# Kernel tuning notes

Hardware: AMD Instinct MI355X
Metric: run time of the kernel (lower is better)

The kernel has to match this reference:

```python
import jax, jax.numpy as jnp
import numpy as np

SOM = (32, 32)   # som_dim; SOM[0]*SOM[1] == num_embeddings
LR = 0.05


def setup_inputs() -> dict:
    key = jax.random.key(0)
    k1, k2 = jax.random.split(key)
    B, K, D = 65536, 1024, 256
    x = jax.random.normal(k1, (B, D), dtype=jnp.float32)
    embeddings = jax.random.uniform(k2, (K, D), dtype=jnp.float32)  # torch.rand init
    return {"x": x, "embeddings": embeddings}


def reference(x, embeddings):
    K, D = embeddings.shape
    # pairwise squared distances: [B, K]
    dist = (jnp.sum(x * x, axis=1, keepdims=True)
            + jnp.sum(embeddings * embeddings, axis=1)
            - 2.0 * (x @ embeddings.T))
    n_min = jnp.argmin(dist, axis=1)          # [B]
    z_q = embeddings[n_min]                   # [B, D]

    # SOM grid coordinates and clamped neighbors
    n_x = n_min // SOM[1]
    n_y = n_min % SOM[1]
    x_up = jnp.where(n_x < SOM[0] - 1, n_x + 1, n_x)
    x_down = jnp.where(n_x > 0, n_x - 1, n_x)
    y_right = jnp.where(n_y < SOM[1] - 1, n_y + 1, n_y)
    y_left = jnp.where(n_y > 0, n_y - 1, n_y)
    idx_up = x_up * SOM[1] + n_y
    idx_down = x_down * SOM[1] + n_y
    idx_right = n_x * SOM[1] + y_right
    idx_left = n_x * SOM[1] + y_left

    # [B, 4, D] neighbor gather (order: up, down, left, right as in torch code)
    nbr_idx = jnp.stack([idx_up, idx_down, idx_left, idx_right], axis=1)
    z_q_neighbors = embeddings[nbr_idx]

    # SOM scatter update (torch does one-hot matmuls; segment_sum is the fused form)
    dw = x - z_q                              # [B, D]
    seg = lambda idx: jax.ops.segment_sum(dw, idx, num_segments=K)
    new_embeddings = jax.lax.stop_gradient(
        embeddings
        + LR * seg(n_min)
        + 0.5 * LR * (seg(idx_up) + seg(idx_down) + seg(idx_right) + seg(idx_left))
    )

    commit_loss = jnp.mean((x - z_q) ** 2)
    som_loss = jnp.mean((jax.lax.stop_gradient(x)[:, None, :] - z_q_neighbors) ** 2)
    return z_q, commit_loss, som_loss, new_embeddings
```

## Files before the change

kernel.cpp:

```cpp
#include <hip/hip_runtime.h>

#define B_ROWS 65536
#define DDIM   256
#define KEMB   1024
#define LRC    0.05f
#define BM 64
#define BN 128

typedef __attribute__((ext_vector_type(8))) _Float16 half8;
typedef __attribute__((ext_vector_type(4))) float f32x4;

#define SX_OFF    0u
#define CNT_OFF   1048576u
#define SUMS_OFF  1052672u
#define ESQ_OFF   1053312u
#define CUR_OFF   1057408u
#define NMIN_OFF  1061504u
#define ROWS_OFF  1585792u
#define EH_OFF    1847936u

static __device__ __forceinline__ unsigned short f2h(float f) {
  _Float16 h = (_Float16)f;
  return *(unsigned short*)&h;
}
static __device__ __forceinline__ float h2f(unsigned short u) {
  _Float16 h = *(_Float16*)&u;
  return (float)h;
}
static __device__ __forceinline__ void glds16(const void* g, void* l) {
  __builtin_amdgcn_global_load_lds(
      (const __attribute__((address_space(1))) unsigned int*)g,
      (__attribute__((address_space(3))) unsigned int*)l, 16, 0, 0);
}

__global__ __launch_bounds__(256) void convert_kernel(
    const float* __restrict__ E, unsigned short* __restrict__ Eh,
    float* __restrict__ esq) {
  size_t i = (size_t)blockIdx.x * 256 + threadIdx.x;
  size_t off = i * 8;
  const float4 v0 = *(const float4*)(E + off);
  const float4 v1 = *(const float4*)(E + off + 4);
  float f[8] = {v0.x, v0.y, v0.z, v0.w, v1.x, v1.y, v1.z, v1.w};
  unsigned short h[8];
  float part = 0.f;
#pragma unroll
  for (int j = 0; j < 8; ++j) {
    h[j] = f2h(f[j]);
    part += f[j] * f[j];
  }
  *(uint4*)(Eh + off) = *(const uint4*)h;
  float s = part;
  for (int o = 16; o > 0; o >>= 1) s += __shfl_down(s, o, 32);
  if ((threadIdx.x & 31) == 0) esq[i >> 5] = s;
}

__global__ __launch_bounds__(256, 2) void gemm_argmin_kernel(
    const float* __restrict__ X, const unsigned short* __restrict__ EhW,
    const float* __restrict__ esq, const float* __restrict__ Ef,
    int* __restrict__ nmin, int* __restrict__ counts, float* __restrict__ zq,
    double* __restrict__ sums) {
  __shared__ __align__(16) unsigned short sX[2][8][256][8];
  __shared__ __align__(16) unsigned short sE[2][512][8];

  const int tid  = threadIdx.x;
  const int lane = tid & 63, w = tid >> 6;
  const int lrow = lane & 15;
  const int qidx = lane >> 4;
  const int rowbase = (w >> 1) * 32;
  const int colb    = (w & 1) * 64;
  const int bm0 = (int)blockIdx.x * BM;

  int ec_row[2], ec_q8[2];
#pragma unroll
  for (int j = 0; j < 2; ++j) {
    const int c = j * 256 + tid;
    ec_row[j] = c >> 2;
    ec_q8[j]  = ((c & 3) ^ ((ec_row[j] >> 1) & 3)) * 8;
  }

#pragma unroll
  for (int j = 0; j < 2; ++j)
    glds16(EhW + (size_t)ec_row[j] * DDIM + ec_q8[j], (char*)&sE[0][j * 256 + tid][0]);

  {
    float part = 0.f;
#pragma unroll
    for (int it = 0; it < 8; ++it) {
      const int c   = it * 256 + tid;
      const int kcc = c >> 8;
      const int cc  = c & 255;
      const int row = cc >> 2;
      const int q   = (cc & 3) ^ ((row >> 1) & 3);
      const float* xp = X + (size_t)(bm0 + row) * DDIM + kcc * 32 + q * 8;
      const float4 a = *(const float4*)xp;
      const float4 b = *(const float4*)(xp + 4);
      float f[8] = {a.x, a.y, a.z, a.w, b.x, b.y, b.z, b.w};
      unsigned short hh[8], ll[8];
#pragma unroll
      for (int m = 0; m < 8; ++m) {
        hh[m] = f2h(f[m]);
        ll[m] = f2h(f[m] - h2f(hh[m]));
        part += f[m] * f[m];
      }
      *(uint4*)((char*)sX + (size_t)c * 16)          = *(const uint4*)hh;
      *(uint4*)((char*)sX + (size_t)(c + 2048) * 16) = *(const uint4*)ll;
    }
#pragma unroll
    for (int o = 32; o > 0; o >>= 1) part += __shfl_down(part, o);
    if (lane == 0)
      atomicAdd(&sums[8 + (((int)blockIdx.x * 4 + w) & 63)], (double)part);
  }

  float rbest[8];
  int   ridx[8];
#pragma unroll
  for (int i = 0; i < 8; ++i) { rbest[i] = 3.4e38f; ridx[i] = 0; }

  int ra[2], rb[4];
#pragma unroll
  for (int t = 0; t < 2; ++t) {
    const int m = rowbase + t * 16 + lrow;
    ra[t] = (m << 2) | (qidx ^ ((m >> 1) & 3));
  }
#pragma unroll
  for (int t = 0; t < 4; ++t) {
    const int n = colb + t * 16 + lrow;
    rb[t] = (n << 2) | (qidx ^ ((n >> 1) & 3));
  }

  __syncthreads();

  for (int nt = 0; nt < 8; ++nt) {
    f32x4 acc[2][4];
#pragma unroll
    for (int i = 0; i < 2; ++i)
#pragma unroll
      for (int j = 0; j < 4; ++j) acc[i][j] = (f32x4){0.f, 0.f, 0.f, 0.f};

#pragma unroll
    for (int kcc = 0; kcc < 8; ++kcc) {
      const int s   = nt * 8 + kcc;
      const int cur = s & 1;
      if (s < 63) {
        const int ns = s + 1;
        const int nnt = ns >> 3, nk = ns & 7;
#pragma unroll
        for (int j = 0; j < 2; ++j) {
          const int c = j * 256 + tid;
          glds16(EhW + (size_t)(nnt * BN + ec_row[j]) * DDIM + nk * 32 + ec_q8[j],
                 (char*)&sE[cur ^ 1][c][0]);
        }
      }
      half8 af0[2], af1[2], bfr[4];
#pragma unroll
      for (int t = 0; t < 2; ++t) {
        af0[t] = *(const half8*)&sX[0][kcc][ra[t]][0];
        af1[t] = *(const half8*)&sX[1][kcc][ra[t]][0];
      }
#pragma unroll
      for (int t = 0; t < 4; ++t) bfr[t] = *(const half8*)&sE[cur][rb[t]][0];
#pragma unroll
      for (int tr = 0; tr < 2; ++tr)
#pragma unroll
        for (int tc = 0; tc < 4; ++tc)
          acc[tr][tc] = __builtin_amdgcn_mfma_f32_16x16x32_f16(
              af0[tr], bfr[tc], acc[tr][tc], 0, 0, 0);
#pragma unroll
      for (int tr = 0; tr < 2; ++tr)
#pragma unroll
        for (int tc = 0; tc < 4; ++tc)
          acc[tr][tc] = __builtin_amdgcn_mfma_f32_16x16x32_f16(
              af1[tr], bfr[tc], acc[tr][tc], 0, 0, 0);
      __syncthreads();
    }
#pragma unroll
    for (int tc = 0; tc < 4; ++tc) {
      const int col = nt * BN + colb + tc * 16 + lrow;
      const float eq = esq[col];
#pragma unroll
      for (int tr = 0; tr < 2; ++tr)
#pragma unroll
        for (int rr = 0; rr < 4; ++rr) {
          float d = eq - 2.0f * acc[tr][tc][rr];
          const int slot = tr * 4 + rr;
          if (d < rbest[slot]) { rbest[slot] = d; ridx[slot] = col; }
        }
    }
  }

  float* cdd = (float*)&sE[0][0][0];
  int*   cdi = (int*)(cdd + 128);
  int*   snm = cdi + 128;
  int*   h   = (int*)&sX[0][0][0][0];

#pragma unroll
  for (int i = 0; i < 4; ++i) h[tid + i * 256] = 0;

#pragma unroll
  for (int slot = 0; slot < 8; ++slot) {
    float bd = rbest[slot];
    int   bi = ridx[slot];
#pragma unroll
    for (int off = 1; off < 16; off <<= 1) {
      float od = __shfl_xor(bd, off, 64);
      int   oi = __shfl_xor(bi, off, 64);
      if (od < bd || (od == bd && oi < bi)) { bd = od; bi = oi; }
    }
    if (lrow == 0) {
      const int row = rowbase + (slot >> 2) * 16 + (lane >> 4) * 4 + (slot & 3);
      cdd[(w & 1) * 64 + row] = bd;
      cdi[(w & 1) * 64 + row] = bi;
    }
  }
  __syncthreads();
  if (tid < BM) {
    float d0 = cdd[tid], d1 = cdd[64 + tid];
    int   i0 = cdi[tid], i1 = cdi[64 + tid];
    int bi = (d1 < d0 || (d1 == d0 && i1 < i0)) ? i1 : i0;
    nmin[bm0 + tid] = bi;
    snm[tid] = bi;
    atomicAdd(&h[bi], 1);
  }
  __syncthreads();
#pragma unroll
  for (int i = 0; i < 4; ++i) {
    int v = h[tid + i * 256];
    if (v) atomicAdd(&counts[tid + i * 256], v);
  }
  const int r0 = w * 16;
#pragma unroll 4
  for (int r = 0; r < 16; ++r) {
    const int k = snm[r0 + r];
    const float4 v = *(const float4*)(Ef + (size_t)k * DDIM + lane * 4);
    *(float4*)(zq + (size_t)(bm0 + r0 + r) * DDIM + lane * 4) = v;
  }
}

__global__ __launch_bounds__(1024) void scan_kernel(
    const int* __restrict__ counts, int* __restrict__ cur) {
  __shared__ int tmp[KEMB];
  int tid = threadIdx.x;
  int v = counts[tid];
  tmp[tid] = v;
  __syncthreads();
  for (int off = 1; off < 1024; off <<= 1) {
    int u = (tid >= off) ? tmp[tid - off] : 0;
    __syncthreads();
    tmp[tid] += u;
    __syncthreads();
  }
  cur[tid] = tmp[tid] - v;
}

__global__ __launch_bounds__(1024) void scatter_kernel(
    const int* __restrict__ nm, int* __restrict__ cur,
    int* __restrict__ rows) {
  __shared__ int lcnt[KEMB], lbase[KEMB], lrank[KEMB];
  int tid = threadIdx.x;
  lcnt[tid] = 0; lrank[tid] = 0;
  __syncthreads();
  int b = blockIdx.x * 1024 + tid;
  int k = nm[b];
  atomicAdd(&lcnt[k], 1);
  __syncthreads();
  if (lcnt[tid] > 0) lbase[tid] = atomicAdd(&cur[tid], lcnt[tid]);
  __syncthreads();
  int r = atomicAdd(&lrank[k], 1);
  rows[lbase[k] + r] = b;
}

__global__ __launch_bounds__(256) void sxsum_kernel(
    const int* __restrict__ rows, const int* __restrict__ nm,
    const float* __restrict__ X, float* __restrict__ SX) {
  __shared__ int sb[32], sk[32];
  int tid = threadIdx.x;
  int p0 = blockIdx.x * 32;
  if (tid < 32) sb[tid] = rows[p0 + tid];
  __syncthreads();
  if (tid < 32) sk[tid] = nm[sb[tid]];
  __syncthreads();
  float acc = 0.f;
  int kprev = sk[0];
  for (int i = 0; i < 32; ++i) {
    int k = sk[i];
    if (k != kprev) {
      atomicAdd(&SX[(size_t)kprev * DDIM + tid], acc);
      acc = 0.f;
      kprev = k;
    }
    acc += X[(size_t)sb[i] * DDIM + tid];
  }
  atomicAdd(&SX[(size_t)kprev * DDIM + tid], acc);
}

__global__ __launch_bounds__(256) void stencil_kernel(
    const float* __restrict__ E, const float* __restrict__ SX,
    const int* __restrict__ counts, const float* __restrict__ esq,
    double* __restrict__ sums, float* __restrict__ out) {
  __shared__ float redc[256], reds[256];
  int k = blockIdx.x, t = threadIdx.x;
  int kx = k >> 5, ky = k & 31;
  int j1 = (kx >= 1)  ? k - 32 : k;
  int j2 = (kx <= 30) ? k + 32 : k;
  int j3 = (ky >= 1)  ? k - 1  : k;
  int j4 = (ky <= 30) ? k + 1  : k;
  int fU = (kx < 31) ? k + 32 : k;
  int fD = (kx > 0)  ? k - 32 : k;
  int fL = (ky > 0)  ? k - 1  : k;
  int fR = (ky < 31) ? k + 1  : k;

  float e   = E[(size_t)k * DDIM + t];
  float sxk = SX[(size_t)k * DDIM + t];
  float Tk = sxk - (float)counts[k] * e;
  float T1 = SX[(size_t)j1 * DDIM + t] - (float)counts[j1] * E[(size_t)j1 * DDIM + t];
  float T2 = SX[(size_t)j2 * DDIM + t] - (float)counts[j2] * E[(size_t)j2 * DDIM + t];
  float T3 = SX[(size_t)j3 * DDIM + t] - (float)counts[j3] * E[(size_t)j3 * DDIM + t];
  float T4 = SX[(size_t)j4 * DDIM + t] - (float)counts[j4] * E[(size_t)j4 * DDIM + t];
  float v = e + LRC * Tk + 0.5f * LRC * (T1 + T2 + T3 + T4);
  out[(size_t)B_ROWS * DDIM + 2 + (size_t)k * DDIM + t] = v;

  float eU = E[(size_t)fU * DDIM + t], eD = E[(size_t)fD * DDIM + t];
  float eL = E[(size_t)fL * DDIM + t], eR = E[(size_t)fR * DDIM + t];
  float cp = -2.f * sxk * e;
  float sp = -2.f * sxk * (eU + eD + eL + eR);
  if (t == 0) {
    float ck = (float)counts[k];
    cp += ck * esq[k];
    sp += ck * (esq[fU] + esq[fD] + esq[fL] + esq[fR]);
  }
  redc[t] = cp; reds[t] = sp;
  __syncthreads();
  for (int s = 128; s > 0; s >>= 1) {
    if (t < s) { redc[t] += redc[t + s]; reds[t] += reds[t + s]; }
    __syncthreads();
  }
  if (t == 0) {
    atomicAdd(&sums[1], (double)redc[0]);
    atomicAdd(&sums[2], (double)reds[0]);
  }
}

__global__ void finalize_kernel(const double* __restrict__ sums,
                                float* __restrict__ out) {
  double xsq = 0.0;
  for (int s = 0; s < 64; ++s) xsq += sums[8 + s];
  out[(size_t)B_ROWS * DDIM]     = (float)((xsq + sums[1]) / ((double)B_ROWS * DDIM));
  out[(size_t)B_ROWS * DDIM + 1] =
      (float)((4.0 * xsq + sums[2]) / ((double)B_ROWS * 4.0 * DDIM));
}

extern "C" void kernel_launch(void* const* d_in, const int* in_sizes, int n_in,
                              void* d_out, int out_size, void* d_ws, size_t ws_size,
                              hipStream_t stream) {
  const float* X = (const float*)d_in[0];
  const float* E = (const float*)d_in[1];
  float* out = (float*)d_out;
  char* ws = (char*)d_ws;

  float*          SX   = (float*)(ws + SX_OFF);
  int*            cnts = (int*)(ws + CNT_OFF);
  double*         sums = (double*)(ws + SUMS_OFF);
  float*          esq  = (float*)(ws + ESQ_OFF);
  int*            cur  = (int*)(ws + CUR_OFF);
  int*            nm   = (int*)(ws + NMIN_OFF);
  int*            rows = (int*)(ws + ROWS_OFF);
  unsigned short* EhW  = (unsigned short*)(ws + EH_OFF);

  hipMemsetAsync(ws, 0, ESQ_OFF, stream);

  convert_kernel<<<KEMB * (DDIM / 8) / 256, 256, 0, stream>>>(E, EhW, esq);
  gemm_argmin_kernel<<<B_ROWS / BM, 256, 0, stream>>>(X, EhW, esq, E, nm, cnts, out,
                                                      sums);
  scan_kernel<<<1, 1024, 0, stream>>>(cnts, cur);
  scatter_kernel<<<B_ROWS / 1024, 1024, 0, stream>>>(nm, cur, rows);
  sxsum_kernel<<<B_ROWS / 32, 256, 0, stream>>>(rows, nm, X, SX);
  stencil_kernel<<<KEMB, 256, 0, stream>>>(E, SX, cnts, esq, sums, out);
  finalize_kernel<<<1, 1, 0, stream>>>(sums, out);
}
```

Before: 250.3 us.

## Widen GEMM N-tile to 512 columns with 32 accumulators per wave

Replaces the 8 passes over 128-column embedding tiles with 2 passes over 512-column tiles. Each wave now holds a 2x16 grid of MFMA accumulators, and the embedding shared buffer grows fourfold. The goal is to cut the number of barriers and k-steps and to reuse the A fragments across more MFMAs. In exchange, occupancy drops to one block per CU (launch bounds 1) and register and LDS pressure rise, which risks spills and less latency hiding.

```diff
diff --git a/kernel.cpp b/kernel.cpp
--- a/kernel.cpp
+++ b/kernel.cpp
@@ -5,7 +5,6 @@
 #define KEMB   1024
 #define LRC    0.05f
 #define BM 64
-#define BN 128
 
 typedef __attribute__((ext_vector_type(8))) _Float16 half8;
 typedef __attribute__((ext_vector_type(4))) float f32x4;
@@ -54,33 +53,29 @@
   if ((threadIdx.x & 31) == 0) esq[i >> 5] = s;
 }
 
-__global__ __launch_bounds__(256, 2) void gemm_argmin_kernel(
+__global__ __launch_bounds__(256, 1) void gemm_argmin_kernel(
     const float* __restrict__ X, const unsigned short* __restrict__ EhW,
     const float* __restrict__ esq, const float* __restrict__ Ef,
     int* __restrict__ nmin, int* __restrict__ counts, float* __restrict__ zq,
     double* __restrict__ sums) {
   __shared__ __align__(16) unsigned short sX[2][8][256][8];
-  __shared__ __align__(16) unsigned short sE[2][512][8];
+  __shared__ __align__(16) unsigned short sE[2][2048][8];
 
   const int tid  = threadIdx.x;
   const int lane = tid & 63, w = tid >> 6;
   const int lrow = lane & 15;
   const int qidx = lane >> 4;
   const int rowbase = (w >> 1) * 32;
-  const int colb    = (w & 1) * 64;
+  const int colb    = (w & 1) * 256;
   const int bm0 = (int)blockIdx.x * BM;
 
-  int ec_row[2], ec_q8[2];
-#pragma unroll
-  for (int j = 0; j < 2; ++j) {
+#pragma unroll
+  for (int j = 0; j < 8; ++j) {
     const int c = j * 256 + tid;
-    ec_row[j] = c >> 2;
-    ec_q8[j]  = ((c & 3) ^ ((ec_row[j] >> 1) & 3)) * 8;
-  }
-
-#pragma unroll
-  for (int j = 0; j < 2; ++j)
-    glds16(EhW + (size_t)ec_row[j] * DDIM + ec_q8[j], (char*)&sE[0][j * 256 + tid][0]);
+    const int row = c >> 2;
+    const int q = (c & 3) ^ ((row >> 1) & 3);
+    glds16(EhW + (size_t)row * DDIM + q * 8, (char*)&sE[0][c][0]);
+  }
 
   {
     float part = 0.f;
@@ -116,66 +111,66 @@
 #pragma unroll
   for (int i = 0; i < 8; ++i) { rbest[i] = 3.4e38f; ridx[i] = 0; }
 
-  int ra[2], rb[4];
+  int ra[2], rbch[16];
 #pragma unroll
   for (int t = 0; t < 2; ++t) {
     const int m = rowbase + t * 16 + lrow;
     ra[t] = (m << 2) | (qidx ^ ((m >> 1) & 3));
   }
 #pragma unroll
-  for (int t = 0; t < 4; ++t) {
-    const int n = colb + t * 16 + lrow;
-    rb[t] = (n << 2) | (qidx ^ ((n >> 1) & 3));
-  }
-
-  __syncthreads();
-
-  for (int nt = 0; nt < 8; ++nt) {
-    f32x4 acc[2][4];
+  for (int tc = 0; tc < 16; ++tc) {
+    const int r = colb + tc * 16 + lrow;
+    rbch[tc] = (r << 2) | (qidx ^ ((r >> 1) & 3));
+  }
+
+  __syncthreads();
+
+#pragma unroll
+  for (int kh = 0; kh < 2; ++kh) {
+    f32x4 acc[2][16];
 #pragma unroll
     for (int i = 0; i < 2; ++i)
 #pragma unroll
-      for (int j = 0; j < 4; ++j) acc[i][j] = (f32x4){0.f, 0.f, 0.f, 0.f};
+      for (int j = 0; j < 16; ++j) acc[i][j] = (f32x4){0.f, 0.f, 0.f, 0.f};
 
 #pragma unroll
     for (int kcc = 0; kcc < 8; ++kcc) {
-      const int s   = nt * 8 + kcc;
-      const int cur = s & 1;
-      if (s < 63) {
-        const int ns = s + 1;
-        const int nnt = ns >> 3, nk = ns & 7;
-#pragma unroll
-        for (int j = 0; j < 2; ++j) {
+      const int p   = kh * 8 + kcc;
+      const int cur = p & 1;
+      if (p + 1 < 16) {
+        const int np = p + 1, nkh = np >> 3, nk = np & 7;
+#pragma unroll
+        for (int j = 0; j < 8; ++j) {
           const int c = j * 256 + tid;
-          glds16(EhW + (size_t)(nnt * BN + ec_row[j]) * DDIM + nk * 32 + ec_q8[j],
+          const int row = c >> 2;
+          const int q = (c & 3) ^ ((row >> 1) & 3);
+          glds16(EhW + (size_t)(nkh * 512 + row) * DDIM + nk * 32 + q * 8,
                  (char*)&sE[cur ^ 1][c][0]);
         }
       }
-      half8 af0[2], af1[2], bfr[4];
+      half8 af0[2], af1[2];
 #pragma unroll
       for (int t = 0; t < 2; ++t) {
         af0[t] = *(const half8*)&sX[0][kcc][ra[t]][0];
         af1[t] = *(const half8*)&sX[1][kcc][ra[t]][0];
       }
 #pragma unroll
-      for (int t = 0; t < 4; ++t) bfr[t] = *(const half8*)&sE[cur][rb[t]][0];
-#pragma unroll
-      for (int tr = 0; tr < 2; ++tr)
-#pragma unroll
-        for (int tc = 0; tc < 4; ++tc)
+      for (int tc = 0; tc < 16; ++tc) {
+        const half8 bfr = *(const half8*)&sE[cur][rbch[tc]][0];
+#pragma unroll
+        for (int tr = 0; tr < 2; ++tr)
           acc[tr][tc] = __builtin_amdgcn_mfma_f32_16x16x32_f16(
-              af0[tr], bfr[tc], acc[tr][tc], 0, 0, 0);
-#pragma unroll
-      for (int tr = 0; tr < 2; ++tr)
-#pragma unroll
-        for (int tc = 0; tc < 4; ++tc)
+              af0[tr], bfr, acc[tr][tc], 0, 0, 0);
+#pragma unroll
+        for (int tr = 0; tr < 2; ++tr)
           acc[tr][tc] = __builtin_amdgcn_mfma_f32_16x16x32_f16(
-              af1[tr], bfr[tc], acc[tr][tc], 0, 0, 0);
+              af1[tr], bfr, acc[tr][tc], 0, 0, 0);
+      }
       __syncthreads();
     }
 #pragma unroll
-    for (int tc = 0; tc < 4; ++tc) {
-      const int col = nt * BN + colb + tc * 16 + lrow;
+    for (int tc = 0; tc < 16; ++tc) {
+      const int col = kh * 512 + colb + tc * 16 + lrow;
       const float eq = esq[col];
 #pragma unroll
       for (int tr = 0; tr < 2; ++tr)
```

After: 291.9 us. 1.17x slower.

## Deepen E-tile prefetch to four buffers and keep X fragments in registers

Applied to the files above, without the earlier changes.

Replaces the double-buffered E tile pipeline with a four-slot ring that prefetches two k-steps ahead. The barrier waits only for older loads via a manual vmcnt wait instead of draining everything. All X fragments are loaded into registers once per block instead of re-reading LDS every step. This raises register and LDS use, so launch bounds drop to one block per SIMD pair, which lowers occupancy. It also relies on hand-tuned waitcnt values being correct.

```diff
diff --git a/kernel.cpp b/kernel.cpp
--- a/kernel.cpp
+++ b/kernel.cpp
@@ -54,13 +54,13 @@
   if ((threadIdx.x & 31) == 0) esq[i >> 5] = s;
 }
 
-__global__ __launch_bounds__(256, 2) void gemm_argmin_kernel(
+__global__ __launch_bounds__(256, 1) void gemm_argmin_kernel(
     const float* __restrict__ X, const unsigned short* __restrict__ EhW,
     const float* __restrict__ esq, const float* __restrict__ Ef,
     int* __restrict__ nmin, int* __restrict__ counts, float* __restrict__ zq,
     double* __restrict__ sums) {
   __shared__ __align__(16) unsigned short sX[2][8][256][8];
-  __shared__ __align__(16) unsigned short sE[2][512][8];
+  __shared__ __align__(16) unsigned short sE[4][512][8];
 
   const int tid  = threadIdx.x;
   const int lane = tid & 63, w = tid >> 6;
@@ -80,7 +80,12 @@
 
 #pragma unroll
   for (int j = 0; j < 2; ++j)
-    glds16(EhW + (size_t)ec_row[j] * DDIM + ec_q8[j], (char*)&sE[0][j * 256 + tid][0]);
+    glds16(EhW + (size_t)ec_row[j] * DDIM + ec_q8[j],
+           (char*)&sE[0][j * 256 + tid][0]);
+#pragma unroll
+  for (int j = 0; j < 2; ++j)
+    glds16(EhW + (size_t)ec_row[j] * DDIM + 32 + ec_q8[j],
+           (char*)&sE[1][j * 256 + tid][0]);
 
   {
     float part = 0.f;
@@ -130,6 +135,15 @@
 
   __syncthreads();
 
+  half8 a0[8][2], a1[8][2];
+#pragma unroll
+  for (int kcc = 0; kcc < 8; ++kcc)
+#pragma unroll
+    for (int t = 0; t < 2; ++t) {
+      a0[kcc][t] = *(const half8*)&sX[0][kcc][ra[t]][0];
+      a1[kcc][t] = *(const half8*)&sX[1][kcc][ra[t]][0];
+    }
+
   for (int nt = 0; nt < 8; ++nt) {
     f32x4 acc[2][4];
 #pragma unroll
@@ -139,39 +153,39 @@
 
 #pragma unroll
     for (int kcc = 0; kcc < 8; ++kcc) {
-      const int s   = nt * 8 + kcc;
-      const int cur = s & 1;
-      if (s < 63) {
-        const int ns = s + 1;
-        const int nnt = ns >> 3, nk = ns & 7;
+      const int s    = nt * 8 + kcc;
+      const int rbuf = kcc & 3;
+      const int wbuf = (kcc + 2) & 3;
+      if (s + 2 < 64) {
+        const int np = s + 2, nnt = np >> 3, nk = np & 7;
 #pragma unroll
         for (int j = 0; j < 2; ++j) {
           const int c = j * 256 + tid;
           glds16(EhW + (size_t)(nnt * BN + ec_row[j]) * DDIM + nk * 32 + ec_q8[j],
-                 (char*)&sE[cur ^ 1][c][0]);
+                 (char*)&sE[wbuf][c][0]);
         }
       }
-      half8 af0[2], af1[2], bfr[4];
-#pragma unroll
-      for (int t = 0; t < 2; ++t) {
-        af0[t] = *(const half8*)&sX[0][kcc][ra[t]][0];
-        af1[t] = *(const half8*)&sX[1][kcc][ra[t]][0];
-      }
-#pragma unroll
-      for (int t = 0; t < 4; ++t) bfr[t] = *(const half8*)&sE[cur][rb[t]][0];
+      half8 bfr[4];
+#pragma unroll
+      for (int t = 0; t < 4; ++t) bfr[t] = *(const half8*)&sE[rbuf][rb[t]][0];
 #pragma unroll
       for (int tr = 0; tr < 2; ++tr)
 #pragma unroll
         for (int tc = 0; tc < 4; ++tc)
           acc[tr][tc] = __builtin_amdgcn_mfma_f32_16x16x32_f16(
-              af0[tr], bfr[tc], acc[tr][tc], 0, 0, 0);
+              a0[kcc][tr], bfr[tc], acc[tr][tc], 0, 0, 0);
 #pragma unroll
       for (int tr = 0; tr < 2; ++tr)
 #pragma unroll
         for (int tc = 0; tc < 4; ++tc)
           acc[tr][tc] = __builtin_amdgcn_mfma_f32_16x16x32_f16(
-              af1[tr], bfr[tc], acc[tr][tc], 0, 0, 0);
-      __syncthreads();
+              a1[kcc][tr], bfr[tc], acc[tr][tc], 0, 0, 0);
+      if (s < 62) {
+        asm volatile("s_waitcnt vmcnt(2)" ::: "memory");
+      } else {
+        asm volatile("s_waitcnt vmcnt(0)" ::: "memory");
+      }
+      __builtin_amdgcn_s_barrier();
     }
 #pragma unroll
     for (int tc = 0; tc < 4; ++tc) {
```

After: 271.9 us. 8.6% more time.
